# Optimization experiments

Hardware: AMD Instinct MI355X
Metric: run time of the kernel (lower is better)

The kernel has to match this reference:

```python
import jax, jax.numpy as jnp
import numpy as np

B, T, D = 2, 2048, 1024
H = 4            # num_heads (== num_kv_heads, num_kv_groups = 1)
W = 512          # window_size
S = 64           # state_size
CK = D // H      # head_k_dim = 256
CV = D // H      # head_v_dim = 256
EPS = 1e-5
SCALE = 1.0


def setup_inputs() -> dict:
    key = jax.random.key(0)
    ks = jax.random.split(key, 8)
    def w(k, o, i):
        return jax.random.normal(k, (o, i), jnp.float32) * 0.02
    return {
        "hidden_states": jax.random.normal(ks[0], (B, T, D), jnp.float32),
        "w_norm": jnp.ones((D,), jnp.float32),   # shared RMSNorm weight (pre- and post-norm; module overwrites self.norm)
        "Wq": w(ks[1], D, D),
        "Wk": w(ks[2], D, D),
        "Wv": w(ks[3], D, D),
        "Ws": w(ks[4], D, D),
        "Wg": w(ks[5], H * S, D),
        "Wo": w(ks[6], D, D),
    }


def _rms(x, w):
    return x * jax.lax.rsqrt(jnp.mean(x * x, axis=-1, keepdims=True) + EPS) * w


def reference(hidden_states, w_norm, Wq, Wk, Wv, Ws, Wg, Wo):
    h = _rms(hidden_states, w_norm)                           # pre-norm (norm_first)
    proj = lambda x, Wm: jnp.einsum('btd,od->bto', x, Wm)
    heads = lambda x, c: x.reshape(B, T, H, c).transpose(0, 2, 1, 3)
    q = heads(proj(h, Wq), CK) * SCALE                        # [B,H,T,CK]
    k = heads(proj(h, Wk), CK)
    v = heads(proj(h, Wv), CV)
    s = heads(proj(h, Ws), CK)                                # state-key projection
    g = jax.nn.softmax(proj(h, Wg), axis=-1)                  # softmax over full H*S dim (as in module)
    g = heads(g, S)                                           # [B,H,T,S] gate over state slots

    # ---- compressed global state (causal cumulative g-weighted outer products) ----
    # state_K[t] = sum_{t'<=t} g[t']^T s[t'];  scores_state[t,s] = q[t] . state_K[t,s]
    causal = jnp.tril(jnp.ones((T, T), dtype=bool))
    A = jnp.einsum('bhtc,bhuc->bhtu', q, s)                   # q . s per pair
    A = jnp.where(causal, A, 0.0)
    sc_state = jnp.einsum('bhtu,bhus->bhts', A, g)            # [B,H,T,S]

    # ---- sliding-window local attention (blocked: each query block sees prev+cur key block) ----
    nb = T // W
    qb = q.reshape(B, H, nb, W, CK)
    kb = k.reshape(B, H, nb, W, CK)
    vb = v.reshape(B, H, nb, W, CV)
    kprev = jnp.concatenate([jnp.zeros_like(kb[:, :, :1]), kb[:, :, :-1]], axis=2)
    vprev = jnp.concatenate([jnp.zeros_like(vb[:, :, :1]), vb[:, :, :-1]], axis=2)
    k2 = jnp.concatenate([kprev, kb], axis=3)                 # [B,H,nb,2W,CK]
    v2 = jnp.concatenate([vprev, vb], axis=3)                 # [B,H,nb,2W,CV]
    sc_w = jnp.einsum('bhnrc,bhnuc->bhnru', qb, k2)           # [B,H,nb,W,2W]

    r = jnp.arange(W)[:, None]
    u = jnp.arange(2 * W)[None, :]
    d = W + r - u                                             # distance t - t_key
    band = (d >= 0) & (d <= W - 1)                            # window of size W, causal
    first_blk = band & (u >= W)                               # block 0 has no real prev block
    wmask = jnp.where(jnp.arange(nb)[:, None, None] == 0, first_blk, band)   # [nb,W,2W]
    slopes = 2.0 ** (-8.0 * jnp.arange(H, dtype=jnp.float32) / H)            # [H]
    bias = -slopes[:, None, None] * d                          # alibi: slopes*(j-W+1) == -slope*dist
    sc_w = sc_w + bias[None, :, None, :, :]
    sc_w = jnp.where(wmask[None, None], sc_w, -1e30)

    # ---- joint softmax over [state ; window] columns ----
    sc = jnp.concatenate([sc_state.reshape(B, H, nb, W, S), sc_w], axis=-1)  # [B,H,nb,W,S+2W]
    p = jax.nn.softmax(sc, axis=-1)
    p_state = p[..., :S].reshape(B, H, T, S)
    p_w = p[..., S:]

    o_w = jnp.einsum('bhnru,bhnuc->bhnrc', p_w, v2).reshape(B, H, T, CV)
    # out_state[t] = sum_s p_state[t,s] * state_V[t,s],  state_V[t] = sum_{t'<=t} g[t']^T v[t']
    M = jnp.einsum('bhts,bhus->bhtu', p_state, g)
    M = jnp.where(causal, M, 0.0)
    o_s = jnp.einsum('bhtu,bhuc->bhtc', M, v)

    o = (o_w + o_s).transpose(0, 2, 1, 3).reshape(B, T, H * CV)
    o = o * jax.nn.sigmoid(o)                                  # swish
    o = _rms(o, w_norm)                                        # rms_norm_linear
    return jnp.einsum('btd,od->bto', o, Wo)
```

## Files before the change

### kernel.cpp

```cpp
#include <hip/hip_runtime.h>
#include <stdint.h>

#define B_  2
#define T_  2048
#define D_  1024
#define H_  4
#define S_  64
#define W_  512
#define CK_ 256
#define NC_ 32

typedef __attribute__((ext_vector_type(8))) short bf16x8;
typedef __attribute__((ext_vector_type(4))) float f32x4;
typedef __attribute__((ext_vector_type(4))) unsigned short u16x4;

__device__ __forceinline__ float bf2f(unsigned short u){ return __uint_as_float(((unsigned int)u)<<16); }
__device__ __forceinline__ unsigned short f2bf(float f){
  unsigned int u = __float_as_uint(f);
  u += 0x7fffu + ((u>>16)&1u);
  return (unsigned short)(u>>16);
}
__device__ __forceinline__ void split2(float y, unsigned short& hi, unsigned short& lo){
  hi = f2bf(y);
  lo = f2bf(y - bf2f(hi));
}

__device__ __forceinline__ void gl_lds16(const unsigned short* g, unsigned short* l){
  __builtin_amdgcn_global_load_lds(
      (const __attribute__((address_space(1))) unsigned int*)g,
      (__attribute__((address_space(3))) unsigned int*)l, 16, 0, 0);
}

__global__ void rmsnorm_split_kernel(const float* __restrict__ x, const float* __restrict__ w,
                                     unsigned short* __restrict__ ohi, unsigned short* __restrict__ olo){
  int row = blockIdx.x, tid = threadIdx.x;
  const float* xr = x + (size_t)row*D_;
  float v0=xr[tid], v1=xr[tid+256], v2=xr[tid+512], v3=xr[tid+768];
  __shared__ float red[256];
  red[tid] = v0*v0+v1*v1+v2*v2+v3*v3;
  __syncthreads();
  for(int s=128;s>0;s>>=1){ if(tid<s) red[tid]+=red[tid+s]; __syncthreads(); }
  float r = rsqrtf(red[0]/(float)D_ + 1e-5f);
  size_t base = (size_t)row*D_;
  float y0=v0*r*w[tid], y1=v1*r*w[tid+256], y2=v2*r*w[tid+512], y3=v3*r*w[tid+768];
  unsigned short hh, ll;
  split2(y0,hh,ll); ohi[base+tid]=hh;     olo[base+tid]=ll;
  split2(y1,hh,ll); ohi[base+tid+256]=hh; olo[base+tid+256]=ll;
  split2(y2,hh,ll); ohi[base+tid+512]=hh; olo[base+tid+512]=ll;
  split2(y3,hh,ll); ohi[base+tid+768]=hh; olo[base+tid+768]=ll;
}

__global__ void wsplit_kernel(const float* __restrict__ Wq, const float* __restrict__ Wk,
                              const float* __restrict__ Ws, const float* __restrict__ Wv,
                              const float* __restrict__ Wg, const float* __restrict__ Wo,
                              unsigned short* __restrict__ whi, unsigned short* __restrict__ wlo){
  int row = blockIdx.x, tid = threadIdx.x;
  const float* src;
  if(row < 1024)      src = Wq + (size_t)row*1024;
  else if(row < 2048) src = Wk + (size_t)(row-1024)*1024;
  else if(row < 3072) src = Ws + (size_t)(row-2048)*1024;
  else if(row < 4096) src = Wv + (size_t)(row-3072)*1024;
  else if(row < 4352) src = Wg + (size_t)(row-4096)*1024;
  else                src = Wo + (size_t)(row-4352)*1024;
  f32x4 vv = *(const f32x4*)(src + tid*4);
  u16x4 hh, ll;
  #pragma unroll
  for(int j=0;j<4;j++){ unsigned short a,b; split2(vv[j],a,b); hh[j]=a; ll[j]=b; }
  *(u16x4*)(whi + (size_t)row*1024 + tid*4) = hh;
  *(u16x4*)(wlo + (size_t)row*1024 + tid*4) = ll;
}

__global__ __launch_bounds__(256,2) void gemm_bf16s(
    const unsigned short* __restrict__ Ahi, const unsigned short* __restrict__ Alo,
    const unsigned short* __restrict__ Whi, const unsigned short* __restrict__ Wlo,
    unsigned short* __restrict__ qks, unsigned short* __restrict__ vt,
    unsigned short* __restrict__ vtlo, float* __restrict__ gout,
    float* __restrict__ Cf, int mode)
{
  __shared__ unsigned short Ah_s[128*64];
  __shared__ unsigned short Al_s[128*64];
  __shared__ unsigned short Bh_s[128*64];
  __shared__ unsigned short Bl_s[128*64];
  int tid = threadIdx.x;
  int lane = tid & 63, w = tid >> 6;
  int quad = lane >> 4, lq = lane & 15;
  int wr = w >> 1, wc = w & 1;
  int bid = blockIdx.y*gridDim.x + blockIdx.x;
  int row0, col0;
  if(mode == 0){
    int xcd = bid & 7, slot = bid >> 3;
    int rx = xcd & 3, cx = xcd >> 2;
    int sr = slot / 17, sc2 = slot % 17;
    row0 = (rx*8 + sr)*128;
    col0 = (cx*17 + sc2)*128;
  } else {
    int q8 = (gridDim.x*gridDim.y) >> 3;
    int wg = (bid & 7)*q8 + (bid >> 3);
    col0 = (wg % gridDim.x)*128;
    row0 = (wg / gridDim.x)*128;
  }

  int l8 = lane >> 3;
  int chk = lane & 7;

  f32x4 acc[4][4];
  #pragma unroll
  for(int i=0;i<4;i++)
    #pragma unroll
    for(int j=0;j<4;j++) acc[i][j] = (f32x4){0.f,0.f,0.f,0.f};

  for(int kt=0; kt<1024; kt+=64){
    __syncthreads();
    #pragma unroll
    for(int j=0;j<4;j++){
      int rl = w*32 + j*8 + l8;
      int sc = (chk ^ (rl & 7))*8;
      int lbase = (w*32 + j*8)*64;
      gl_lds16(Ahi + (size_t)(row0+rl)*1024 + kt + sc, Ah_s + lbase);
      gl_lds16(Alo + (size_t)(row0+rl)*1024 + kt + sc, Al_s + lbase);
      gl_lds16(Whi + (size_t)(col0+rl)*1024 + kt + sc, Bh_s + lbase);
      gl_lds16(Wlo + (size_t)(col0+rl)*1024 + kt + sc, Bl_s + lbase);
    }
    __syncthreads();
    #pragma unroll
    for(int ks=0;ks<2;ks++){
      bf16x8 afh[4], afl[4], bfh[4], bfl[4];
      #pragma unroll
      for(int i=0;i<4;i++){
        int Ra = wr*64+i*16+lq;
        int ca = ((ks*4+quad) ^ (Ra&7))*8;
        afh[i] = *(const bf16x8*)(const void*)(Ah_s + Ra*64 + ca);
        afl[i] = *(const bf16x8*)(const void*)(Al_s + Ra*64 + ca);
        int Rb = wc*64+i*16+lq;
        int cb = ((ks*4+quad) ^ (Rb&7))*8;
        bfh[i] = *(const bf16x8*)(const void*)(Bh_s + Rb*64 + cb);
        bfl[i] = *(const bf16x8*)(const void*)(Bl_s + Rb*64 + cb);
      }
      #pragma unroll
      for(int mi=0;mi<4;mi++)
        #pragma unroll
        for(int ni=0;ni<4;ni++){
          acc[mi][ni] = __builtin_amdgcn_mfma_f32_16x16x32_bf16(afh[mi], bfh[ni], acc[mi][ni], 0,0,0);
          acc[mi][ni] = __builtin_amdgcn_mfma_f32_16x16x32_bf16(afh[mi], bfl[ni], acc[mi][ni], 0,0,0);
          acc[mi][ni] = __builtin_amdgcn_mfma_f32_16x16x32_bf16(afl[mi], bfh[ni], acc[mi][ni], 0,0,0);
        }
    }
  }

  int rbase = row0 + wr*64, cbase = col0 + wc*64;
  if(mode == 1){
    #pragma unroll
    for(int mi=0;mi<4;mi++)
      #pragma unroll
      for(int ni=0;ni<4;ni++)
        #pragma unroll
        for(int i=0;i<4;i++)
          Cf[(size_t)(rbase+mi*16+quad*4+i)*1024 + cbase+ni*16+lq] = acc[mi][ni][i];
  } else if(col0 < 3072){
    unsigned short* dst = qks + (size_t)(col0>>10)*4194304;
    #pragma unroll
    for(int mi=0;mi<4;mi++)
      #pragma unroll
      for(int ni=0;ni<4;ni++)
        #pragma unroll
        for(int i=0;i<4;i++){
          int rr = rbase+mi*16+quad*4+i, cc = (cbase+ni*16+lq) & 1023;
          dst[(size_t)rr*1024 + cc] = f2bf(acc[mi][ni][i]);
        }
  } else if(col0 < 4096){
    #pragma unroll
    for(int mi=0;mi<4;mi++)
      #pragma unroll
      for(int ni=0;ni<4;ni++)
        #pragma unroll
        for(int i=0;i<4;i++){
          int rr = rbase+mi*16+quad*4+i, cl = (cbase+ni*16+lq) & 1023;
          unsigned short hh2, ll2;
          split2(acc[mi][ni][i], hh2, ll2);
          int hh = cl>>8, cv = cl&255, bb = rr>>11, tt = rr&2047;
          size_t ti = ((size_t)((bb*H_+hh)*256 + cv))*T_ + tt;
          vt[ti] = hh2;
          vtlo[ti] = ll2;
        }
  } else {
    #pragma unroll
    for(int mi=0;mi<4;mi++)
      #pragma unroll
      for(int ni=0;ni<4;ni++)
        #pragma unroll
        for(int i=0;i<4;i++){
          int rr = rbase+mi*16+quad*4+i, cl = cbase+ni*16+lq - 4096;
          gout[(size_t)rr*256 + cl] = acc[mi][ni][i];
        }
  }
}

__global__ void softmax256_kernel(float* __restrict__ g){
  int row = blockIdx.x, tid = threadIdx.x;
  float x = g[(size_t)row*256+tid];
  __shared__ float red[256];
  red[tid]=x; __syncthreads();
  for(int s=128;s>0;s>>=1){ if(tid<s) red[tid]=fmaxf(red[tid],red[tid+s]); __syncthreads(); }
  float m = red[0]; __syncthreads();
  float e = expf(x-m);
  red[tid]=e; __syncthreads();
  for(int s=128;s>0;s>>=1){ if(tid<s) red[tid]+=red[tid+s]; __syncthreads(); }
  g[(size_t)row*256+tid] = e/red[0];
}

__global__ __launch_bounds__(256,1) void chunk_outer_mfma(
    const unsigned short* __restrict__ gthi, const unsigned short* __restrict__ gtlo,
    const unsigned short* __restrict__ s_bf, float* __restrict__ out)
{
  __shared__ unsigned short xh_lds[256*72];
  int n=blockIdx.x, h=blockIdx.y, b=blockIdx.z;
  int tid=threadIdx.x, lane=tid&63, w=tid>>6;
  int quad=lane>>4, lq=lane&15;
  int t0=n*64, bh=b*H_+h;

  const unsigned short* sb = s_bf + (size_t)(b*T_+t0)*D_ + h*CK_ + tid;
  for(int p2=0;p2<8;p2++){
    union{ unsigned short u[8]; bf16x8 v8; } r8;
    #pragma unroll
    for(int j=0;j<8;j++)
      r8.u[j] = sb[(size_t)(p2*8+j)*D_];
    *(bf16x8*)(void*)&xh_lds[tid*72 + p2*8] = r8.v8;
  }
  __syncthreads();

  size_t gtbase = ((size_t)bh*NC_ + n)*64;
  f32x4 acc[4][4];
  #pragma unroll
  for(int i=0;i<4;i++)
    #pragma unroll
    for(int j=0;j<4;j++) acc[i][j] = (f32x4){0.f,0.f,0.f,0.f};

  #pragma unroll
  for(int ks=0; ks<2; ks++){
    bf16x8 ah[4], al[4], bh4[4];
    #pragma unroll
    for(int mi=0;mi<4;mi++){
      ah[mi] = *(const bf16x8*)(const void*)(gthi + (gtbase + mi*16+lq)*64 + ks*32 + quad*8);
      al[mi] = *(const bf16x8*)(const void*)(gtlo + (gtbase + mi*16+lq)*64 + ks*32 + quad*8);
    }
    #pragma unroll
    for(int ni=0;ni<4;ni++)
      bh4[ni] = *(const bf16x8*)(const void*)&xh_lds[(w*64+ni*16+lq)*72 + ks*32 + quad*8];
    #pragma unroll
    for(int mi=0;mi<4;mi++)
      #pragma unroll
      for(int ni=0;ni<4;ni++){
        acc[mi][ni] = __builtin_amdgcn_mfma_f32_16x16x32_bf16(ah[mi], bh4[ni], acc[mi][ni], 0,0,0);
        acc[mi][ni] = __builtin_amdgcn_mfma_f32_16x16x32_bf16(al[mi], bh4[ni], acc[mi][ni], 0,0,0);
      }
  }
  size_t obase = ((size_t)bh*NC_ + n)*16384;
  #pragma unroll
  for(int mi=0;mi<4;mi++)
    #pragma unroll
    for(int ni=0;ni<4;ni++)
      #pragma unroll
      for(int i=0;i<4;i++){
        int s = mi*16 + quad*4 + i, c = w*64 + ni*16 + lq;
        out[obase + (size_t)s*256 + c] = acc[mi][ni][i];
      }
}

__global__ __launch_bounds__(256,1) void chunk_outer_vt(
    const unsigned short* __restrict__ gthi, const unsigned short* __restrict__ gtlo,
    const unsigned short* __restrict__ vt, const unsigned short* __restrict__ vtlo,
    float* __restrict__ out)
{
  int n=blockIdx.x, h=blockIdx.y, b=blockIdx.z;
  int tid=threadIdx.x, lane=tid&63, w=tid>>6;
  int quad=lane>>4, lq=lane&15;
  int t0=n*64, bh=b*H_+h;
  size_t gtbase = ((size_t)bh*NC_ + n)*64;
  f32x4 acc[4][4];
  #pragma unroll
  for(int i=0;i<4;i++)
    #pragma unroll
    for(int j=0;j<4;j++) acc[i][j] = (f32x4){0.f,0.f,0.f,0.f};

  #pragma unroll
  for(int ks=0; ks<2; ks++){
    bf16x8 ah[4], al[4];
    #pragma unroll
    for(int mi=0;mi<4;mi++){
      ah[mi] = *(const bf16x8*)(const void*)(gthi + (gtbase + mi*16+lq)*64 + ks*32 + quad*8);
      al[mi] = *(const bf16x8*)(const void*)(gtlo + (gtbase + mi*16+lq)*64 + ks*32 + quad*8);
    }
    #pragma unroll
    for(int ni=0;ni<4;ni++){
      size_t vo = ((size_t)(bh*256 + w*64 + ni*16 + lq))*T_ + t0 + ks*32 + quad*8;
      bf16x8 vh = *(const bf16x8*)(const void*)(vt + vo);
      bf16x8 vl = *(const bf16x8*)(const void*)(vtlo + vo);
      #pragma unroll
      for(int mi=0;mi<4;mi++){
        acc[mi][ni] = __builtin_amdgcn_mfma_f32_16x16x32_bf16(ah[mi], vh, acc[mi][ni], 0,0,0);
        acc[mi][ni] = __builtin_amdgcn_mfma_f32_16x16x32_bf16(al[mi], vh, acc[mi][ni], 0,0,0);
        acc[mi][ni] = __builtin_amdgcn_mfma_f32_16x16x32_bf16(ah[mi], vl, acc[mi][ni], 0,0,0);
      }
    }
  }
  size_t obase = ((size_t)bh*NC_ + n)*16384;
  #pragma unroll
  for(int mi=0;mi<4;mi++)
    #pragma unroll
    for(int ni=0;ni<4;ni++){
      int c = w*64 + ni*16 + lq, s0 = mi*16 + quad*4;
      *(f32x4*)&out[obase + (size_t)c*64 + s0] = acc[mi][ni];
    }
}

__global__ void chunk_prefix_split_kernel(const float* __restrict__ arr,
    unsigned short* __restrict__ hi, unsigned short* __restrict__ lo){
  int idx = blockIdx.x*256 + threadIdx.x;
  int bh = idx >> 14, e = idx & 16383;
  float run = 0.f;
  size_t base = (size_t)bh*NC_*16384 + e;
  for(int n=0;n<NC_;n++){
    size_t a = base + (size_t)n*16384;
    float t = arr[a];
    unsigned short hh, ll;
    split2(run, hh, ll);
    hi[a] = hh; lo[a] = ll;
    run += t;
  }
}

__global__ __launch_bounds__(256) void g_transpose_split_kernel(const float* __restrict__ g,
    unsigned short* __restrict__ gthi, unsigned short* __restrict__ gtlo){
  int n=blockIdx.x, h=blockIdx.y, b=blockIdx.z;
  int tid=threadIdx.x, t0=n*64;
  __shared__ float tt[64][65];
  #pragma unroll
  for(int p=0;p<16;p++){
    int u = (tid>>6) + p*4, s = tid&63;
    tt[s][u] = g[((size_t)(b*T_ + t0 + u))*256 + h*64 + s];
  }
  __syncthreads();
  size_t base = ((size_t)(b*H_+h)*NC_ + n)*64;
  #pragma unroll
  for(int p=0;p<16;p++){
    int s = (tid>>6) + p*4, u = tid&63;
    unsigned short hh, ll;
    split2(tt[s][u], hh, ll);
    gthi[(base+s)*64 + u] = hh;
    gtlo[(base+s)*64 + u] = ll;
  }
}

__global__ __launch_bounds__(256,1) void sc_state_mfma(
    const unsigned short* __restrict__ q_bf,
    const unsigned short* __restrict__ s_bf,
    const unsigned short* __restrict__ S1hi, const unsigned short* __restrict__ S1lo,
    const unsigned short* __restrict__ gthi, const unsigned short* __restrict__ gtlo,
    float* __restrict__ sc_state)
{
  int n=blockIdx.x, h=blockIdx.y, b=blockIdx.z;
  int tid=threadIdx.x, lane=tid&63, w=tid>>6;
  int quad=lane>>4, lq=lane&15;
  int t0=n*64, bh=b*H_+h, strip=w*16;

  __shared__ unsigned short A_hi[64*72];
  __shared__ unsigned short A_lo[64*72];

  bf16x8 qf[8];
  const unsigned short* qrow = q_bf + ((size_t)(b*T_ + t0 + strip + lq))*D_ + h*CK_ + quad*8;
  #pragma unroll
  for(int ks=0;ks<8;ks++) qf[ks] = *(const bf16x8*)(const void*)(qrow + ks*32);

  const unsigned short* sbase = s_bf + ((size_t)(b*T_ + t0))*D_ + h*CK_;
  f32x4 a1[4];
  #pragma unroll
  for(int nf=0;nf<4;nf++) a1[nf] = (f32x4){0.f,0.f,0.f,0.f};
  #pragma unroll
  for(int ks=0;ks<8;ks++){
    #pragma unroll
    for(int nf=0;nf<4;nf++){
      bf16x8 sf = *(const bf16x8*)(const void*)(sbase + (size_t)(nf*16+lq)*D_ + ks*32 + quad*8);
      a1[nf] = __builtin_amdgcn_mfma_f32_16x16x32_bf16(qf[ks], sf, a1[nf], 0,0,0);
    }
  }
  #pragma unroll
  for(int nf=0;nf<4;nf++){
    int u = nf*16 + lq;
    #pragma unroll
    for(int i=0;i<4;i++){
      int trow = strip + quad*4 + i;
      float val = (u <= trow) ? a1[nf][i] : 0.f;
      unsigned short hh, ll;
      split2(val, hh, ll);
      A_hi[trow*72 + u] = hh;
      A_lo[trow*72 + u] = ll;
    }
  }
  __syncthreads();

  bf16x8 afh[2], afl[2];
  #pragma unroll
  for(int ks=0;ks<2;ks++){
    afh[ks] = *(const bf16x8*)(const void*)&A_hi[(strip+lq)*72 + ks*32 + quad*8];
    afl[ks] = *(const bf16x8*)(const void*)&A_lo[(strip+lq)*72 + ks*32 + quad*8];
  }

  size_t s1base = ((size_t)bh*NC_ + n)*16384;
  size_t gtbase = ((size_t)bh*NC_ + n)*64;
  f32x4 acc2[4];
  #pragma unroll
  for(int nf=0;nf<4;nf++) acc2[nf] = (f32x4){0.f,0.f,0.f,0.f};
  #pragma unroll
  for(int ks=0;ks<8;ks++){
    #pragma unroll
    for(int nf=0;nf<4;nf++){
      size_t off = s1base + (size_t)(nf*16+lq)*256 + ks*32 + quad*8;
      bf16x8 b1 = *(const bf16x8*)(const void*)(S1hi + off);
      acc2[nf] = __builtin_amdgcn_mfma_f32_16x16x32_bf16(qf[ks], b1, acc2[nf], 0,0,0);
      bf16x8 b2 = *(const bf16x8*)(const void*)(S1lo + off);
      acc2[nf] = __builtin_amdgcn_mfma_f32_16x16x32_bf16(qf[ks], b2, acc2[nf], 0,0,0);
    }
  }
  #pragma unroll
  for(int ks=0;ks<2;ks++){
    #pragma unroll
    for(int nf=0;nf<4;nf++){
      size_t off = (gtbase + nf*16+lq)*64 + ks*32 + quad*8;
      bf16x8 gh = *(const bf16x8*)(const void*)(gthi + off);
      bf16x8 gl = *(const bf16x8*)(const void*)(gtlo + off);
      acc2[nf] = __builtin_amdgcn_mfma_f32_16x16x32_bf16(afh[ks], gh, acc2[nf], 0,0,0);
      acc2[nf] = __builtin_amdgcn_mfma_f32_16x16x32_bf16(afh[ks], gl, acc2[nf], 0,0,0);
      acc2[nf] = __builtin_amdgcn_mfma_f32_16x16x32_bf16(afl[ks], gh, acc2[nf], 0,0,0);
    }
  }
  #pragma unroll
  for(int nf=0;nf<4;nf++){
    #pragma unroll
    for(int i=0;i<4;i++){
      int trow = strip + quad*4 + i;
      sc_state[((size_t)bh*T_ + t0 + trow)*64 + nf*16+lq] = acc2[nf][i];
    }
  }
}

__global__ __launch_bounds__(256,1) void window_attn_mfma(
    const unsigned short* __restrict__ q_bf,
    const unsigned short* __restrict__ k_bf,
    const unsigned short* __restrict__ vt_bf,
    const float* __restrict__ sc_state,
    float* __restrict__ o,
    unsigned short* __restrict__ phi, unsigned short* __restrict__ plo)
{
  int nt=blockIdx.x, h=blockIdx.y, b=blockIdx.z;
  int tid=threadIdx.x;
  int lane = tid & 63, w = tid >> 6;
  int quad = lane >> 4, lq = lane & 15;
  int sp = w >> 1, np = w & 1;
  int t0 = nt*64, bh = b*H_ + h;
  float slope = exp2f(-2.0f*(float)h);

  __shared__ unsigned short kv_lds[256*72];
  __shared__ float S_lds[64*68];
  __shared__ unsigned short P_lds[64*72];
  __shared__ float m_lds[64], l_lds[64], al_lds[64];

  bf16x8 qf[2][8];
  #pragma unroll
  for(int st=0; st<2; st++){
    const unsigned short* qrow = q_bf + ((size_t)(b*T_ + t0 + 32*sp + 16*st + lq))*D_ + h*CK_ + quad*8;
    #pragma unroll
    for(int ks=0; ks<8; ks++)
      qf[st][ks] = *(const bf16x8*)(const void*)(qrow + ks*32);
  }

  int jt0 = (nt>=8)? nt-8 : 0;
  int krow = tid>>2, kseg = tid&3;
  bf16x8 kpre[8];
  {
    const unsigned short* src = k_bf + ((size_t)(b*T_ + jt0*64 + krow))*D_ + h*CK_ + kseg*64;
    #pragma unroll
    for(int i=0;i<8;i++) kpre[i] = *(const bf16x8*)(const void*)(src + i*8);
  }

  int r = tid >> 2, part = tid & 3;
  {
    const float* scrow = sc_state + ((size_t)bh*T_ + t0 + r)*64 + part*16;
    float pm = -1e30f, sv[16];
    #pragma unroll
    for(int i=0;i<16;i++){ sv[i] = scrow[i]; pm = fmaxf(pm, sv[i]); }
    pm = fmaxf(pm, __shfl_xor(pm,1)); pm = fmaxf(pm, __shfl_xor(pm,2));
    float ps = 0.f;
    #pragma unroll
    for(int i=0;i<16;i++) ps += __expf(sv[i]-pm);
    ps += __shfl_xor(ps,1); ps += __shfl_xor(ps,2);
    if(part==0){ m_lds[r]=pm; l_lds[r]=ps; }
  }

  f32x4 o_acc[2][8];
  #pragma unroll
  for(int st=0;st<2;st++)
    #pragma unroll
    for(int nv=0;nv<8;nv++) o_acc[st][nv] = (f32x4){0.f,0.f,0.f,0.f};
  __syncthreads();

  for(int jt=jt0; jt<=nt; jt++){
    int j0 = jt*64;
    {
      unsigned short* dst = kv_lds + krow*260 + kseg*64;
      #pragma unroll
      for(int i=0;i<8;i++) *(bf16x8*)(void*)(dst + i*8) = kpre[i];
    }
    __syncthreads();
    if(jt < nt){
      const unsigned short* src = k_bf + ((size_t)(b*T_ + j0 + 64 + krow))*D_ + h*CK_ + kseg*64;
      #pragma unroll
      for(int i=0;i<8;i++) kpre[i] = *(const bf16x8*)(const void*)(src + i*8);
    }
    f32x4 sacc[2][2];
    #pragma unroll
    for(int st=0;st<2;st++)
      #pragma unroll
      for(int n2=0;n2<2;n2++) sacc[st][n2] = (f32x4){0.f,0.f,0.f,0.f};
    #pragma unroll
    for(int n2=0;n2<2;n2++){
      int n = np*2 + n2;
      #pragma unroll
      for(int ks=0;ks<8;ks++){
        bf16x8 kf = *(const bf16x8*)(const void*)(kv_lds + (n*16+lq)*260 + ks*32 + quad*8);
        sacc[0][n2] = __builtin_amdgcn_mfma_f32_16x16x32_bf16(qf[0][ks], kf, sacc[0][n2], 0,0,0);
        sacc[1][n2] = __builtin_amdgcn_mfma_f32_16x16x32_bf16(qf[1][ks], kf, sacc[1][n2], 0,0,0);
      }
    }
    #pragma unroll
    for(int st=0;st<2;st++){
      #pragma unroll
      for(int n2=0;n2<2;n2++){
        int n = np*2+n2;
        int u = j0 + n*16 + lq;
        #pragma unroll
        for(int i=0;i<4;i++){
          int row = 32*sp + 16*st + quad*4 + i;
          int d = (t0 + row) - u;
          float val = (d>=0 && d<W_) ? sacc[st][n2][i] - slope*(float)d : -1e30f;
          S_lds[row*68 + n*16+lq] = val;
        }
      }
    }
    __syncthreads();
    {
      float s16[16], tm = -1e30f;
      #pragma unroll
      for(int i=0;i<16;i++){ s16[i] = S_lds[r*68 + part*16 + i]; tm = fmaxf(tm, s16[i]); }
      tm = fmaxf(tm, __shfl_xor(tm,1)); tm = fmaxf(tm, __shfl_xor(tm,2));
      float m_old = m_lds[r];
      float m_new = fmaxf(m_old, tm);
      float alpha = __expf(m_old - m_new);
      float ts = 0.f;
      union { unsigned short u[16]; bf16x8 v[2]; } pk;
      #pragma unroll
      for(int i=0;i<16;i++){ float p = __expf(s16[i]-m_new); ts += p; pk.u[i] = f2bf(p); }
      ts += __shfl_xor(ts,1); ts += __shfl_xor(ts,2);
      *(bf16x8*)(void*)&P_lds[r*72 + part*16]     = pk.v[0];
      *(bf16x8*)(void*)&P_lds[r*72 + part*16 + 8] = pk.v[1];
      if(part==0){ m_lds[r] = m_new; l_lds[r] = l_lds[r]*alpha + ts; al_lds[r] = alpha; }
      #pragma unroll
      for(int pass=0; pass<4; pass++){
        int cv = (tid>>2) + 64*pass, useg = (tid&3)*16;
        const unsigned short* src = vt_bf + ((size_t)(bh*256 + cv))*T_ + j0 + useg;
        unsigned short* dst = kv_lds + cv*72 + useg;
        *(bf16x8*)(void*)(dst)   = *(const bf16x8*)(const void*)(src);
        *(bf16x8*)(void*)(dst+8) = *(const bf16x8*)(const void*)(src+8);
      }
    }
    __syncthreads();
    #pragma unroll
    for(int st=0;st<2;st++){
      #pragma unroll
      for(int i=0;i<4;i++){
        float al = al_lds[32*sp+16*st+quad*4+i];
        #pragma unroll
        for(int nv=0;nv<8;nv++) o_acc[st][nv][i] *= al;
      }
    }
    bf16x8 pa[2][2];
    #pragma unroll
    for(int st=0;st<2;st++)
      #pragma unroll
      for(int k2=0;k2<2;k2++)
        pa[st][k2] = *(const bf16x8*)(const void*)&P_lds[(32*sp+16*st+lq)*72 + k2*32 + quad*8];
    #pragma unroll
    for(int nv=0;nv<8;nv++){
      int cvt = np*8 + nv;
      #pragma unroll
      for(int k2=0;k2<2;k2++){
        bf16x8 vb = *(const bf16x8*)(const void*)(kv_lds + (cvt*16+lq)*72 + k2*32 + quad*8);
        o_acc[0][nv] = __builtin_amdgcn_mfma_f32_16x16x32_bf16(pa[0][k2], vb, o_acc[0][nv], 0,0,0);
        o_acc[1][nv] = __builtin_amdgcn_mfma_f32_16x16x32_bf16(pa[1][k2], vb, o_acc[1][nv], 0,0,0);
      }
    }
    __syncthreads();
  }
  #pragma unroll
  for(int st=0;st<2;st++){
    #pragma unroll
    for(int i=0;i<4;i++){
      int row = 32*sp+16*st+quad*4+i;
      float rl = 1.0f / l_lds[row];
      #pragma unroll
      for(int nv=0;nv<8;nv++){
        int cv = (np*8+nv)*16 + lq;
        o[((size_t)bh*T_ + t0 + row)*256 + cv] = o_acc[st][nv][i] * rl;
      }
    }
  }
  {
    float mf = m_lds[r], rlf = 1.0f / l_lds[r];
    const float* scrow = sc_state + ((size_t)bh*T_ + t0 + r)*64 + part*16;
    size_t pb = ((size_t)bh*T_ + t0 + r)*64 + part*16;
    #pragma unroll
    for(int i=0;i<16;i++){
      float pv = __expf(scrow[i]-mf)*rlf;
      unsigned short hh, ll;
      split2(pv, hh, ll);
      phi[pb+i] = hh;
      plo[pb+i] = ll;
    }
  }
}

__global__ __launch_bounds__(256,1) void o_state_mfma(
    const unsigned short* __restrict__ phi, const unsigned short* __restrict__ plo,
    const float* __restrict__ g,
    const unsigned short* __restrict__ S2hi, const unsigned short* __restrict__ S2lo,
    const unsigned short* __restrict__ vt, const unsigned short* __restrict__ vtlo,
    float* __restrict__ o)
{
  __shared__ unsigned short gh_lds[64*72];
  __shared__ unsigned short gl_lds[64*72];
  __shared__ unsigned short Mh_lds[64*72];
  __shared__ unsigned short Ml_lds[64*72];
  int n=blockIdx.x, h=blockIdx.y, b=blockIdx.z;
  int tid=threadIdx.x, lane=tid&63, w=tid>>6;
  int quad=lane>>4, lq=lane&15;
  int t0=n*64, bh=b*H_+h, strip=w*16;

  {
    int gu = tid>>2, gs0 = (tid&3)*16;
    const float* gr = g + ((size_t)(b*T_+t0+gu))*256 + h*64 + gs0;
    union{ unsigned short u[16]; bf16x8 v[2]; } GH, GL;
    #pragma unroll
    for(int j=0;j<16;j++) split2(gr[j], GH.u[j], GL.u[j]);
    *(bf16x8*)(void*)&gh_lds[gu*72+gs0]   = GH.v[0];
    *(bf16x8*)(void*)&gh_lds[gu*72+gs0+8] = GH.v[1];
    *(bf16x8*)(void*)&gl_lds[gu*72+gs0]   = GL.v[0];
    *(bf16x8*)(void*)&gl_lds[gu*72+gs0+8] = GL.v[1];
  }
  __syncthreads();

  {
    const unsigned short* ph = phi + ((size_t)bh*T_ + t0 + strip + lq)*64;
    const unsigned short* pl = plo + ((size_t)bh*T_ + t0 + strip + lq)*64;
    f32x4 ma[4];
    #pragma unroll
    for(int nf=0;nf<4;nf++) ma[nf] = (f32x4){0.f,0.f,0.f,0.f};
    #pragma unroll
    for(int ks=0;ks<2;ks++){
      bf16x8 pfh = *(const bf16x8*)(const void*)(ph + ks*32 + quad*8);
      bf16x8 pfl = *(const bf16x8*)(const void*)(pl + ks*32 + quad*8);
      #pragma unroll
      for(int nf=0;nf<4;nf++){
        bf16x8 gH = *(const bf16x8*)(const void*)&gh_lds[(nf*16+lq)*72 + ks*32 + quad*8];
        bf16x8 gL = *(const bf16x8*)(const void*)&gl_lds[(nf*16+lq)*72 + ks*32 + quad*8];
        ma[nf] = __builtin_amdgcn_mfma_f32_16x16x32_bf16(pfh, gH, ma[nf], 0,0,0);
        ma[nf] = __builtin_amdgcn_mfma_f32_16x16x32_bf16(pfh, gL, ma[nf], 0,0,0);
        ma[nf] = __builtin_amdgcn_mfma_f32_16x16x32_bf16(pfl, gH, ma[nf], 0,0,0);
      }
    }
    #pragma unroll
    for(int nf=0;nf<4;nf++){
      int u = nf*16 + lq;
      #pragma unroll
      for(int i=0;i<4;i++){
        int trow = strip + quad*4 + i;
        float val = (u <= trow) ? ma[nf][i] : 0.f;
        unsigned short hh, ll;
        split2(val, hh, ll);
        Mh_lds[trow*72 + u] = hh;
        Ml_lds[trow*72 + u] = ll;
      }
    }
  }
  __syncthreads();

  f32x4 oacc[4][4];
  #pragma unroll
  for(int i=0;i<4;i++)
    #pragma unroll
    for(int j=0;j<4;j++) oacc[i][j] = (f32x4){0.f,0.f,0.f,0.f};
  int c0 = w*64;
  size_t sgbase = ((size_t)bh*NC_ + n)*16384;
  #pragma unroll
  for(int ks=0;ks<2;ks++){
    bf16x8 pAh[4], pAl[4], mAh[4], mAl[4];
    #pragma unroll
    for(int mi=0;mi<4;mi++){
      size_t po = ((size_t)bh*T_ + t0 + mi*16+lq)*64 + ks*32 + quad*8;
      pAh[mi] = *(const bf16x8*)(const void*)(phi + po);
      pAl[mi] = *(const bf16x8*)(const void*)(plo + po);
      mAh[mi] = *(const bf16x8*)(const void*)&Mh_lds[(mi*16+lq)*72 + ks*32 + quad*8];
      mAl[mi] = *(const bf16x8*)(const void*)&Ml_lds[(mi*16+lq)*72 + ks*32 + quad*8];
    }
    #pragma unroll
    for(int ni=0;ni<4;ni++){
      int c = c0 + ni*16 + lq;
      size_t so = sgbase + (size_t)c*64 + ks*32 + quad*8;
      bf16x8 sgH = *(const bf16x8*)(const void*)(S2hi + so);
      bf16x8 sgL = *(const bf16x8*)(const void*)(S2lo + so);
      size_t vo = ((size_t)(bh*256 + c))*T_ + t0 + ks*32 + quad*8;
      bf16x8 vH = *(const bf16x8*)(const void*)(vt + vo);
      bf16x8 vL = *(const bf16x8*)(const void*)(vtlo + vo);
      #pragma unroll
      for(int mi=0;mi<4;mi++){
        oacc[mi][ni] = __builtin_amdgcn_mfma_f32_16x16x32_bf16(pAh[mi], sgH, oacc[mi][ni], 0,0,0);
        oacc[mi][ni] = __builtin_amdgcn_mfma_f32_16x16x32_bf16(pAh[mi], sgL, oacc[mi][ni], 0,0,0);
        oacc[mi][ni] = __builtin_amdgcn_mfma_f32_16x16x32_bf16(pAl[mi], sgH, oacc[mi][ni], 0,0,0);
        oacc[mi][ni] = __builtin_amdgcn_mfma_f32_16x16x32_bf16(mAh[mi], vH, oacc[mi][ni], 0,0,0);
        oacc[mi][ni] = __builtin_amdgcn_mfma_f32_16x16x32_bf16(mAl[mi], vH, oacc[mi][ni], 0,0,0);
        oacc[mi][ni] = __builtin_amdgcn_mfma_f32_16x16x32_bf16(mAh[mi], vL, oacc[mi][ni], 0,0,0);
      }
    }
  }
  #pragma unroll
  for(int mi=0;mi<4;mi++)
    #pragma unroll
    for(int ni=0;ni<4;ni++)
      #pragma unroll
      for(int i=0;i<4;i++){
        int trow = mi*16 + quad*4 + i, c = c0 + ni*16 + lq;
        size_t oi = ((size_t)bh*T_ + t0 + trow)*256 + c;
        o[oi] += oacc[mi][ni][i];
      }
}

__global__ void swish_rms_split_kernel(const float* __restrict__ o, const float* __restrict__ w,
                                       unsigned short* __restrict__ ohi, unsigned short* __restrict__ olo){
  int bt=blockIdx.x, tid=threadIdx.x;
  int b = bt >> 11, t = bt & 2047;
  float y[4]; float ss=0.f;
  #pragma unroll
  for(int hh=0;hh<4;hh++){
    float x = o[((size_t)(b*H_+hh)*T_ + t)*256 + tid];
    float yy = x / (1.f + expf(-x));
    y[hh]=yy; ss += yy*yy;
  }
  __shared__ float red[256];
  red[tid]=ss; __syncthreads();
  for(int s2=128;s2>0;s2>>=1){ if(tid<s2) red[tid]+=red[tid+s2]; __syncthreads(); }
  float r = rsqrtf(red[0]/1024.f + 1e-5f);
  #pragma unroll
  for(int hh=0;hh<4;hh++){
    unsigned short a,bq;
    split2(y[hh]*r*w[hh*256+tid], a, bq);
    ohi[(size_t)bt*1024 + hh*256 + tid] = a;
    olo[(size_t)bt*1024 + hh*256 + tid] = bq;
  }
}

extern "C" void kernel_launch(void* const* d_in, const int* in_sizes, int n_in,
                              void* d_out, int out_size, void* d_ws, size_t ws_size,
                              hipStream_t stream){
  const float* hidden = (const float*)d_in[0];
  const float* w_norm = (const float*)d_in[1];
  const float* Wq = (const float*)d_in[2];
  const float* Wk = (const float*)d_in[3];
  const float* Wv = (const float*)d_in[4];
  const float* Ws = (const float*)d_in[5];
  const float* Wg = (const float*)d_in[6];
  const float* Wo = (const float*)d_in[7];
  float* out = (float*)d_out;

  char* p = (char*)d_ws;
  auto alloc = [&](size_t bytes)->void*{ void* r = (void*)p; p += (bytes + 255) & ~(size_t)255; return r; };
  unsigned short* h_hi = (unsigned short*)alloc(8388608);
  unsigned short* h_lo = (unsigned short*)alloc(8388608);
  unsigned short* Wc_hi = (unsigned short*)alloc(11010048);
  unsigned short* Wc_lo = (unsigned short*)alloc(11010048);
  unsigned short* vslot = (unsigned short*)alloc(16777216);
  float* g   = (float*)alloc(4194304);
  float* P1  = (float*)alloc(16777216);
  float* P2  = (float*)alloc(16777216);
  float* sc  = (float*)alloc(4194304);
  float* ps  = (float*)alloc(4194304);
  unsigned short* qks = (unsigned short*)alloc(25165824);
  unsigned short* vt  = (unsigned short*)alloc(8388608);

  unsigned short* vtlo = vslot;
  unsigned short* S2hi = vslot + 4194304;
  unsigned short* q_bf = qks;
  unsigned short* k_bf = qks + 4194304;
  unsigned short* s_bf = qks + 8388608;
  unsigned short* S2lo = s_bf;
  float* o = P1;
  unsigned short* S1hi = (unsigned short*)P2;
  unsigned short* S1lo = S1hi + 4194304;
  unsigned short* GThi = (unsigned short*)ps;
  unsigned short* GTlo = GThi + 1048576;
  unsigned short* phi  = (unsigned short*)ps;
  unsigned short* plo  = phi + 1048576;

  rmsnorm_split_kernel<<<4096,256,0,stream>>>(hidden, w_norm, h_hi, h_lo);
  wsplit_kernel<<<5376,256,0,stream>>>(Wq, Wk, Ws, Wv, Wg, Wo, Wc_hi, Wc_lo);
  gemm_bf16s<<<dim3(34,32),256,0,stream>>>(h_hi, h_lo, Wc_hi, Wc_lo,
                                           qks, vt, vtlo, g, nullptr, 0);
  softmax256_kernel<<<4096,256,0,stream>>>(g);
  dim3 gc(32,4,2);
  g_transpose_split_kernel<<<gc,256,0,stream>>>(g, GThi, GTlo);
  chunk_outer_mfma<<<gc,256,0,stream>>>(GThi, GTlo, s_bf, P1);
  chunk_prefix_split_kernel<<<512,256,0,stream>>>(P1, S1hi, S1lo);
  sc_state_mfma<<<gc,256,0,stream>>>(q_bf, s_bf, S1hi, S1lo, GThi, GTlo, sc);
  chunk_outer_vt<<<gc,256,0,stream>>>(GThi, GTlo, vt, vtlo, P2);
  chunk_prefix_split_kernel<<<512,256,0,stream>>>(P2, S2hi, S2lo);
  window_attn_mfma<<<gc,256,0,stream>>>(q_bf, k_bf, vt, sc, o, phi, plo);
  o_state_mfma<<<gc,256,0,stream>>>(phi, plo, g, S2hi, S2lo, vt, vtlo, o);
  swish_rms_split_kernel<<<4096,256,0,stream>>>(o, w_norm, h_hi, h_lo);
  gemm_bf16s<<<dim3(8,32),256,0,stream>>>(h_hi, h_lo, Wc_hi + (size_t)4352*1024, Wc_lo + (size_t)4352*1024,
                                          nullptr, nullptr, nullptr, nullptr, out, 1);
}
```

Before: 384.6 us.

## Fuse pre-norm/weight split, softmax/transpose, chunk outers, and window/state output kernels

Merges the RMSNorm and weight-split kernels into one launch, folds the gate transpose and hi/lo split into the softmax kernel, and computes both chunk outer products (s and v) in a single kernel. The state-output computation moves into the window-attention kernel, so the state probabilities stay in LDS and are added to the window accumulators in registers instead of going through a global round trip and a read-modify-write of o. This removes several launches and intermediate global buffers, at the cost of much more LDS per block in the fused attention kernel and a strided, uncoalesced transposed store from the softmax kernel.

```diff
diff --git a/kernel.cpp b/kernel.cpp
--- a/kernel.cpp
+++ b/kernel.cpp
@@ -31,43 +31,45 @@
       (__attribute__((address_space(3))) unsigned int*)l, 16, 0, 0);
 }
 
-__global__ void rmsnorm_split_kernel(const float* __restrict__ x, const float* __restrict__ w,
-                                     unsigned short* __restrict__ ohi, unsigned short* __restrict__ olo){
-  int row = blockIdx.x, tid = threadIdx.x;
-  const float* xr = x + (size_t)row*D_;
-  float v0=xr[tid], v1=xr[tid+256], v2=xr[tid+512], v3=xr[tid+768];
-  __shared__ float red[256];
-  red[tid] = v0*v0+v1*v1+v2*v2+v3*v3;
-  __syncthreads();
-  for(int s=128;s>0;s>>=1){ if(tid<s) red[tid]+=red[tid+s]; __syncthreads(); }
-  float r = rsqrtf(red[0]/(float)D_ + 1e-5f);
-  size_t base = (size_t)row*D_;
-  float y0=v0*r*w[tid], y1=v1*r*w[tid+256], y2=v2*r*w[tid+512], y3=v3*r*w[tid+768];
-  unsigned short hh, ll;
-  split2(y0,hh,ll); ohi[base+tid]=hh;     olo[base+tid]=ll;
-  split2(y1,hh,ll); ohi[base+tid+256]=hh; olo[base+tid+256]=ll;
-  split2(y2,hh,ll); ohi[base+tid+512]=hh; olo[base+tid+512]=ll;
-  split2(y3,hh,ll); ohi[base+tid+768]=hh; olo[base+tid+768]=ll;
-}
-
-__global__ void wsplit_kernel(const float* __restrict__ Wq, const float* __restrict__ Wk,
-                              const float* __restrict__ Ws, const float* __restrict__ Wv,
-                              const float* __restrict__ Wg, const float* __restrict__ Wo,
-                              unsigned short* __restrict__ whi, unsigned short* __restrict__ wlo){
-  int row = blockIdx.x, tid = threadIdx.x;
-  const float* src;
-  if(row < 1024)      src = Wq + (size_t)row*1024;
-  else if(row < 2048) src = Wk + (size_t)(row-1024)*1024;
-  else if(row < 3072) src = Ws + (size_t)(row-2048)*1024;
-  else if(row < 4096) src = Wv + (size_t)(row-3072)*1024;
-  else if(row < 4352) src = Wg + (size_t)(row-4096)*1024;
-  else                src = Wo + (size_t)(row-4352)*1024;
-  f32x4 vv = *(const f32x4*)(src + tid*4);
-  u16x4 hh, ll;
-  #pragma unroll
-  for(int j=0;j<4;j++){ unsigned short a,b; split2(vv[j],a,b); hh[j]=a; ll[j]=b; }
-  *(u16x4*)(whi + (size_t)row*1024 + tid*4) = hh;
-  *(u16x4*)(wlo + (size_t)row*1024 + tid*4) = ll;
+__global__ void norm_wsplit_kernel(const float* __restrict__ x, const float* __restrict__ w,
+                                   unsigned short* __restrict__ ohi, unsigned short* __restrict__ olo,
+                                   const float* __restrict__ Wq, const float* __restrict__ Wk,
+                                   const float* __restrict__ Ws, const float* __restrict__ Wv,
+                                   const float* __restrict__ Wg, const float* __restrict__ Wo,
+                                   unsigned short* __restrict__ whi, unsigned short* __restrict__ wlo){
+  int tid = threadIdx.x;
+  if(blockIdx.x < 4096){
+    int row = blockIdx.x;
+    const float* xr = x + (size_t)row*D_;
+    float v0=xr[tid], v1=xr[tid+256], v2=xr[tid+512], v3=xr[tid+768];
+    __shared__ float red[256];
+    red[tid] = v0*v0+v1*v1+v2*v2+v3*v3;
+    __syncthreads();
+    for(int s=128;s>0;s>>=1){ if(tid<s) red[tid]+=red[tid+s]; __syncthreads(); }
+    float r = rsqrtf(red[0]/(float)D_ + 1e-5f);
+    size_t base = (size_t)row*D_;
+    float y0=v0*r*w[tid], y1=v1*r*w[tid+256], y2=v2*r*w[tid+512], y3=v3*r*w[tid+768];
+    unsigned short hh, ll;
+    split2(y0,hh,ll); ohi[base+tid]=hh;     olo[base+tid]=ll;
+    split2(y1,hh,ll); ohi[base+tid+256]=hh; olo[base+tid+256]=ll;
+    split2(y2,hh,ll); ohi[base+tid+512]=hh; olo[base+tid+512]=ll;
+    split2(y3,hh,ll); ohi[base+tid+768]=hh; olo[base+tid+768]=ll;
+  } else {
+    int row = blockIdx.x - 4096;
+    const float* src;
+    if(row < 1024)      src = Wq + (size_t)row*1024;
+    else if(row < 2048) src = Wk + (size_t)(row-1024)*1024;
+    else if(row < 3072) src = Ws + (size_t)(row-2048)*1024;
+    else if(row < 4096) src = Wv + (size_t)(row-3072)*1024;
+    else if(row < 4352) src = Wg + (size_t)(row-4096)*1024;
+    else                src = Wo + (size_t)(row-4352)*1024;
+    f32x4 vv = *(const f32x4*)(src + tid*4);
+    u16x4 hh, ll;
+    #pragma unroll
+    for(int j=0;j<4;j++){ unsigned short a,b2; split2(vv[j],a,b2); hh[j]=a; ll[j]=b2; }
+    *(u16x4*)(whi + (size_t)row*1024 + tid*4) = hh;
+    *(u16x4*)(wlo + (size_t)row*1024 + tid*4) = ll;
+  }
 }
 
 __global__ __launch_bounds__(256,2) void gemm_bf16s(
@@ -195,7 +197,8 @@
   }
 }
 
-__global__ void softmax256_kernel(float* __restrict__ g){
+__global__ void softmax256_gt_kernel(float* __restrict__ g,
+    unsigned short* __restrict__ gthi, unsigned short* __restrict__ gtlo){
   int row = blockIdx.x, tid = threadIdx.x;
   float x = g[(size_t)row*256+tid];
   __shared__ float red[256];
@@ -205,18 +208,31 @@
   float e = expf(x-m);
   red[tid]=e; __syncthreads();
   for(int s=128;s>0;s>>=1){ if(tid<s) red[tid]+=red[tid+s]; __syncthreads(); }
-  g[(size_t)row*256+tid] = e/red[0];
-}
-
-__global__ __launch_bounds__(256,1) void chunk_outer_mfma(
+  float val = e/red[0];
+  g[(size_t)row*256+tid] = val;
+  int b = row >> 11, t = row & 2047;
+  int n = t >> 6, u = t & 63;
+  int hsel = tid >> 6, s = tid & 63;
+  unsigned short hh, ll;
+  split2(val, hh, ll);
+  size_t base = ((size_t)(b*H_+hsel)*NC_ + n)*64;
+  gthi[(base+s)*64 + u] = hh;
+  gtlo[(base+s)*64 + u] = ll;
+}
+
+__global__ __launch_bounds__(256,1) void chunk_outer_both(
     const unsigned short* __restrict__ gthi, const unsigned short* __restrict__ gtlo,
-    const unsigned short* __restrict__ s_bf, float* __restrict__ out)
+    const unsigned short* __restrict__ s_bf,
+    const unsigned short* __restrict__ vt, const unsigned short* __restrict__ vtlo,
+    float* __restrict__ outS, float* __restrict__ outV)
 {
   __shared__ unsigned short xh_lds[256*72];
   int n=blockIdx.x, h=blockIdx.y, b=blockIdx.z;
   int tid=threadIdx.x, lane=tid&63, w=tid>>6;
   int quad=lane>>4, lq=lane&15;
   int t0=n*64, bh=b*H_+h;
+  size_t gtbase = ((size_t)bh*NC_ + n)*64;
+  size_t obase = ((size_t)bh*NC_ + n)*16384;
 
   const unsigned short* sb = s_bf + (size_t)(b*T_+t0)*D_ + h*CK_ + tid;
   for(int p2=0;p2<8;p2++){
@@ -228,13 +244,11 @@
   }
   __syncthreads();
 
-  size_t gtbase = ((size_t)bh*NC_ + n)*64;
   f32x4 acc[4][4];
   #pragma unroll
   for(int i=0;i<4;i++)
     #pragma unroll
     for(int j=0;j<4;j++) acc[i][j] = (f32x4){0.f,0.f,0.f,0.f};
-
   #pragma unroll
   for(int ks=0; ks<2; ks++){
     bf16x8 ah[4], al[4], bh4[4];
@@ -254,7 +268,6 @@
         acc[mi][ni] = __builtin_amdgcn_mfma_f32_16x16x32_bf16(al[mi], bh4[ni], acc[mi][ni], 0,0,0);
       }
   }
-  size_t obase = ((size_t)bh*NC_ + n)*16384;
   #pragma unroll
   for(int mi=0;mi<4;mi++)
     #pragma unroll
@@ -262,26 +275,13 @@
       #pragma unroll
       for(int i=0;i<4;i++){
         int s = mi*16 + quad*4 + i, c = w*64 + ni*16 + lq;
-        out[obase + (size_t)s*256 + c] = acc[mi][ni][i];
-      }
-}
-
-__global__ __launch_bounds__(256,1) void chunk_outer_vt(
-    const unsigned short* __restrict__ gthi, const unsigned short* __restrict__ gtlo,
-    const unsigned short* __restrict__ vt, const unsigned short* __restrict__ vtlo,
-    float* __restrict__ out)
-{
-  int n=blockIdx.x, h=blockIdx.y, b=blockIdx.z;
-  int tid=threadIdx.x, lane=tid&63, w=tid>>6;
-  int quad=lane>>4, lq=lane&15;
-  int t0=n*64, bh=b*H_+h;
-  size_t gtbase = ((size_t)bh*NC_ + n)*64;
-  f32x4 acc[4][4];
+        outS[obase + (size_t)s*256 + c] = acc[mi][ni][i];
+      }
+
   #pragma unroll
   for(int i=0;i<4;i++)
     #pragma unroll
     for(int j=0;j<4;j++) acc[i][j] = (f32x4){0.f,0.f,0.f,0.f};
-
   #pragma unroll
   for(int ks=0; ks<2; ks++){
     bf16x8 ah[4], al[4];
@@ -303,13 +303,12 @@
       }
     }
   }
-  size_t obase = ((size_t)bh*NC_ + n)*16384;
   #pragma unroll
   for(int mi=0;mi<4;mi++)
     #pragma unroll
     for(int ni=0;ni<4;ni++){
       int c = w*64 + ni*16 + lq, s0 = mi*16 + quad*4;
-      *(f32x4*)&out[obase + (size_t)c*64 + s0] = acc[mi][ni];
+      *(f32x4*)&outV[obase + (size_t)c*64 + s0] = acc[mi][ni];
     }
 }
 
@@ -329,28 +328,6 @@
   }
 }
 
-__global__ __launch_bounds__(256) void g_transpose_split_kernel(const float* __restrict__ g,
-    unsigned short* __restrict__ gthi, unsigned short* __restrict__ gtlo){
-  int n=blockIdx.x, h=blockIdx.y, b=blockIdx.z;
-  int tid=threadIdx.x, t0=n*64;
-  __shared__ float tt[64][65];
-  #pragma unroll
-  for(int p=0;p<16;p++){
-    int u = (tid>>6) + p*4, s = tid&63;
-    tt[s][u] = g[((size_t)(b*T_ + t0 + u))*256 + h*64 + s];
-  }
-  __syncthreads();
-  size_t base = ((size_t)(b*H_+h)*NC_ + n)*64;
-  #pragma unroll
-  for(int p=0;p<16;p++){
-    int s = (tid>>6) + p*4, u = tid&63;
-    unsigned short hh, ll;
-    split2(tt[s][u], hh, ll);
-    gthi[(base+s)*64 + u] = hh;
-    gtlo[(base+s)*64 + u] = ll;
-  }
-}
-
 __global__ __launch_bounds__(256,1) void sc_state_mfma(
     const unsigned short* __restrict__ q_bf,
     const unsigned short* __restrict__ s_bf,
@@ -443,13 +420,15 @@
   }
 }
 
-__global__ __launch_bounds__(256,1) void window_attn_mfma(
+__global__ __launch_bounds__(256,1) void window_attn_state_mfma(
     const unsigned short* __restrict__ q_bf,
     const unsigned short* __restrict__ k_bf,
     const unsigned short* __restrict__ vt_bf,
+    const unsigned short* __restrict__ vtlo_bf,
     const float* __restrict__ sc_state,
-    float* __restrict__ o,
-    unsigned short* __restrict__ phi, unsigned short* __restrict__ plo)
+    const float* __restrict__ g,
+    const unsigned short* __restrict__ S2hi, const unsigned short* __restrict__ S2lo,
+    float* __restrict__ o)
 {
   int nt=blockIdx.x, h=blockIdx.y, b=blockIdx.z;
   int tid=threadIdx.x;
@@ -462,6 +441,11 @@
   __shared__ unsigned short kv_lds[256*72];
   __shared__ float S_lds[64*68];
   __shared__ unsigned short P_lds[64*72];
+  __shared__ unsigned short Pl_lds[64*72];
+  __shared__ unsigned short gh_lds[64*72];
+  __shared__ unsigned short gl_lds[64*72];
+  __shared__ unsigned short Mh_lds[64*72];
+  __shared__ unsigned short Ml_lds[64*72];
   __shared__ float m_lds[64], l_lds[64], al_lds[64];
 
   bf16x8 qf[2][8];
@@ -600,50 +584,30 @@
     }
     __syncthreads();
   }
-  #pragma unroll
-  for(int st=0;st<2;st++){
+
+  #pragma unroll
+  for(int st=0;st<2;st++)
     #pragma unroll
     for(int i=0;i<4;i++){
       int row = 32*sp+16*st+quad*4+i;
       float rl = 1.0f / l_lds[row];
       #pragma unroll
-      for(int nv=0;nv<8;nv++){
-        int cv = (np*8+nv)*16 + lq;
-        o[((size_t)bh*T_ + t0 + row)*256 + cv] = o_acc[st][nv][i] * rl;
-      }
-    }
-  }
+      for(int nv=0;nv<8;nv++) o_acc[st][nv][i] *= rl;
+    }
   {
     float mf = m_lds[r], rlf = 1.0f / l_lds[r];
     const float* scrow = sc_state + ((size_t)bh*T_ + t0 + r)*64 + part*16;
-    size_t pb = ((size_t)bh*T_ + t0 + r)*64 + part*16;
+    union { unsigned short u[16]; bf16x8 v[2]; } PH, PL;
     #pragma unroll
     for(int i=0;i<16;i++){
       float pv = __expf(scrow[i]-mf)*rlf;
-      unsigned short hh, ll;
-      split2(pv, hh, ll);
-      phi[pb+i] = hh;
-      plo[pb+i] = ll;
-    }
-  }
-}
-
-__global__ __launch_bounds__(256,1) void o_state_mfma(
-    const unsigned short* __restrict__ phi, const unsigned short* __restrict__ plo,
-    const float* __restrict__ g,
-    const unsigned short* __restrict__ S2hi, const unsigned short* __restrict__ S2lo,
-    const unsigned short* __restrict__ vt, const unsigned short* __restrict__ vtlo,
-    float* __restrict__ o)
-{
-  __shared__ unsigned short gh_lds[64*72];
-  __shared__ unsigned short gl_lds[64*72];
-  __shared__ unsigned short Mh_lds[64*72];
-  __shared__ unsigned short Ml_lds[64*72];
-  int n=blockIdx.x, h=blockIdx.y, b=blockIdx.z;
-  int tid=threadIdx.x, lane=tid&63, w=tid>>6;
-  int quad=lane>>4, lq=lane&15;
-  int t0=n*64, bh=b*H_+h, strip=w*16;
-
+      split2(pv, PH.u[i], PL.u[i]);
+    }
+    *(bf16x8*)(void*)&P_lds[r*72 + part*16]      = PH.v[0];
+    *(bf16x8*)(void*)&P_lds[r*72 + part*16 + 8]  = PH.v[1];
+    *(bf16x8*)(void*)&Pl_lds[r*72 + part*16]     = PL.v[0];
+    *(bf16x8*)(void*)&Pl_lds[r*72 + part*16 + 8] = PL.v[1];
+  }
   {
     int gu = tid>>2, gs0 = (tid&3)*16;
     const float* gr = g + ((size_t)(b*T_+t0+gu))*256 + h*64 + gs0;
@@ -658,15 +622,14 @@
   __syncthreads();
 
   {
-    const unsigned short* ph = phi + ((size_t)bh*T_ + t0 + strip + lq)*64;
-    const unsigned short* pl = plo + ((size_t)bh*T_ + t0 + strip + lq)*64;
+    int strip = w*16;
     f32x4 ma[4];
     #pragma unroll
     for(int nf=0;nf<4;nf++) ma[nf] = (f32x4){0.f,0.f,0.f,0.f};
     #pragma unroll
     for(int ks=0;ks<2;ks++){
-      bf16x8 pfh = *(const bf16x8*)(const void*)(ph + ks*32 + quad*8);
-      bf16x8 pfl = *(const bf16x8*)(const void*)(pl + ks*32 + quad*8);
+      bf16x8 pfh = *(const bf16x8*)(const void*)&P_lds[(strip+lq)*72 + ks*32 + quad*8];
+      bf16x8 pfl = *(const bf16x8*)(const void*)&Pl_lds[(strip+lq)*72 + ks*32 + quad*8];
       #pragma unroll
       for(int nf=0;nf<4;nf++){
         bf16x8 gH = *(const bf16x8*)(const void*)&gh_lds[(nf*16+lq)*72 + ks*32 + quad*8];
@@ -692,54 +655,50 @@
   }
   __syncthreads();
 
-  f32x4 oacc[4][4];
-  #pragma unroll
-  for(int i=0;i<4;i++)
-    #pragma unroll
-    for(int j=0;j<4;j++) oacc[i][j] = (f32x4){0.f,0.f,0.f,0.f};
-  int c0 = w*64;
-  size_t sgbase = ((size_t)bh*NC_ + n)*16384;
+  size_t sgbase = ((size_t)bh*NC_ + nt)*16384;
   #pragma unroll
   for(int ks=0;ks<2;ks++){
-    bf16x8 pAh[4], pAl[4], mAh[4], mAl[4];
-    #pragma unroll
-    for(int mi=0;mi<4;mi++){
-      size_t po = ((size_t)bh*T_ + t0 + mi*16+lq)*64 + ks*32 + quad*8;
-      pAh[mi] = *(const bf16x8*)(const void*)(phi + po);
-      pAl[mi] = *(const bf16x8*)(const void*)(plo + po);
-      mAh[mi] = *(const bf16x8*)(const void*)&Mh_lds[(mi*16+lq)*72 + ks*32 + quad*8];
-      mAl[mi] = *(const bf16x8*)(const void*)&Ml_lds[(mi*16+lq)*72 + ks*32 + quad*8];
-    }
-    #pragma unroll
-    for(int ni=0;ni<4;ni++){
-      int c = c0 + ni*16 + lq;
+    bf16x8 pAh[2], pAl[2], mAh[2], mAl[2];
+    #pragma unroll
+    for(int st=0;st<2;st++){
+      int rowb = (32*sp + 16*st + lq)*72 + ks*32 + quad*8;
+      pAh[st] = *(const bf16x8*)(const void*)&P_lds[rowb];
+      pAl[st] = *(const bf16x8*)(const void*)&Pl_lds[rowb];
+      mAh[st] = *(const bf16x8*)(const void*)&Mh_lds[rowb];
+      mAl[st] = *(const bf16x8*)(const void*)&Ml_lds[rowb];
+    }
+    #pragma unroll
+    for(int nv=0;nv<8;nv++){
+      int c = (np*8+nv)*16 + lq;
       size_t so = sgbase + (size_t)c*64 + ks*32 + quad*8;
       bf16x8 sgH = *(const bf16x8*)(const void*)(S2hi + so);
       bf16x8 sgL = *(const bf16x8*)(const void*)(S2lo + so);
       size_t vo = ((size_t)(bh*256 + c))*T_ + t0 + ks*32 + quad*8;
-      bf16x8 vH = *(const bf16x8*)(const void*)(vt + vo);
-      bf16x8 vL = *(const bf16x8*)(const void*)(vtlo + vo);
-      #pragma unroll
-      for(int mi=0;mi<4;mi++){
-        oacc[mi][ni] = __builtin_amdgcn_mfma_f32_16x16x32_bf16(pAh[mi], sgH, oacc[mi][ni], 0,0,0);
-        oacc[mi][ni] = __builtin_amdgcn_mfma_f32_16x16x32_bf16(pAh[mi], sgL, oacc[mi][ni], 0,0,0);
-        oacc[mi][ni] = __builtin_amdgcn_mfma_f32_16x16x32_bf16(pAl[mi], sgH, oacc[mi][ni], 0,0,0);
-        oacc[mi][ni] = __builtin_amdgcn_mfma_f32_16x16x32_bf16(mAh[mi], vH, oacc[mi][ni], 0,0,0);
-        oacc[mi][ni] = __builtin_amdgcn_mfma_f32_16x16x32_bf16(mAl[mi], vH, oacc[mi][ni], 0,0,0);
-        oacc[mi][ni] = __builtin_amdgcn_mfma_f32_16x16x32_bf16(mAh[mi], vL, oacc[mi][ni], 0,0,0);
-      }
-    }
-  }
-  #pragma unroll
-  for(int mi=0;mi<4;mi++)
-    #pragma unroll
-    for(int ni=0;ni<4;ni++)
-      #pragma unroll
-      for(int i=0;i<4;i++){
-        int trow = mi*16 + quad*4 + i, c = c0 + ni*16 + lq;
-        size_t oi = ((size_t)bh*T_ + t0 + trow)*256 + c;
-        o[oi] += oacc[mi][ni][i];
-      }
+      bf16x8 vH = *(const bf16x8*)(const void*)(vt_bf + vo);
+      bf16x8 vL = *(const bf16x8*)(const void*)(vtlo_bf + vo);
+      #pragma unroll
+      for(int st=0;st<2;st++){
+        o_acc[st][nv] = __builtin_amdgcn_mfma_f32_16x16x32_bf16(pAh[st], sgH, o_acc[st][nv], 0,0,0);
+        o_acc[st][nv] = __builtin_amdgcn_mfma_f32_16x16x32_bf16(pAh[st], sgL, o_acc[st][nv], 0,0,0);
+        o_acc[st][nv] = __builtin_amdgcn_mfma_f32_16x16x32_bf16(pAl[st], sgH, o_acc[st][nv], 0,0,0);
+        o_acc[st][nv] = __builtin_amdgcn_mfma_f32_16x16x32_bf16(mAh[st], vH, o_acc[st][nv], 0,0,0);
+        o_acc[st][nv] = __builtin_amdgcn_mfma_f32_16x16x32_bf16(mAl[st], vH, o_acc[st][nv], 0,0,0);
+        o_acc[st][nv] = __builtin_amdgcn_mfma_f32_16x16x32_bf16(mAh[st], vL, o_acc[st][nv], 0,0,0);
+      }
+    }
+  }
+  #pragma unroll
+  for(int st=0;st<2;st++){
+    #pragma unroll
+    for(int i=0;i<4;i++){
+      int row = 32*sp+16*st+quad*4+i;
+      #pragma unroll
+      for(int nv=0;nv<8;nv++){
+        int cv = (np*8+nv)*16 + lq;
+        o[((size_t)bh*T_ + t0 + row)*256 + cv] = o_acc[st][nv][i];
+      }
+    }
+  }
 }
 
 __global__ void swish_rms_split_kernel(const float* __restrict__ o, const float* __restrict__ w,
@@ -801,27 +760,23 @@
   unsigned short* s_bf = qks + 8388608;
   unsigned short* S2lo = s_bf;
   float* o = P1;
+  float* P2f = (float*)h_hi;
   unsigned short* S1hi = (unsigned short*)P2;
   unsigned short* S1lo = S1hi + 4194304;
   unsigned short* GThi = (unsigned short*)ps;
   unsigned short* GTlo = GThi + 1048576;
-  unsigned short* phi  = (unsigned short*)ps;
-  unsigned short* plo  = phi + 1048576;
-
-  rmsnorm_split_kernel<<<4096,256,0,stream>>>(hidden, w_norm, h_hi, h_lo);
-  wsplit_kernel<<<5376,256,0,stream>>>(Wq, Wk, Ws, Wv, Wg, Wo, Wc_hi, Wc_lo);
+
+  norm_wsplit_kernel<<<9472,256,0,stream>>>(hidden, w_norm, h_hi, h_lo,
+                                            Wq, Wk, Ws, Wv, Wg, Wo, Wc_hi, Wc_lo);
   gemm_bf16s<<<dim3(34,32),256,0,stream>>>(h_hi, h_lo, Wc_hi, Wc_lo,
                                            qks, vt, vtlo, g, nullptr, 0);
-  softmax256_kernel<<<4096,256,0,stream>>>(g);
+  softmax256_gt_kernel<<<4096,256,0,stream>>>(g, GThi, GTlo);
   dim3 gc(32,4,2);
-  g_transpose_split_kernel<<<gc,256,0,stream>>>(g, GThi, GTlo);
-  chunk_outer_mfma<<<gc,256,0,stream>>>(GThi, GTlo, s_bf, P1);
+  chunk_outer_both<<<gc,256,0,stream>>>(GThi, GTlo, s_bf, vt, vtlo, P1, P2f);
   chunk_prefix_split_kernel<<<512,256,0,stream>>>(P1, S1hi, S1lo);
   sc_state_mfma<<<gc,256,0,stream>>>(q_bf, s_bf, S1hi, S1lo, GThi, GTlo, sc);
-  chunk_outer_vt<<<gc,256,0,stream>>>(GThi, GTlo, vt, vtlo, P2);
-  chunk_prefix_split_kernel<<<512,256,0,stream>>>(P2, S2hi, S2lo);
-  window_attn_mfma<<<gc,256,0,stream>>>(q_bf, k_bf, vt, sc, o, phi, plo);
-  o_state_mfma<<<gc,256,0,stream>>>(phi, plo, g, S2hi, S2lo, vt, vtlo, o);
+  chunk_prefix_split_kernel<<<512,256,0,stream>>>(P2f, S2hi, S2lo);
+  window_attn_state_mfma<<<gc,256,0,stream>>>(q_bf, k_bf, vt, vtlo, sc, g, S2hi, S2lo, o);
   swish_rms_split_kernel<<<4096,256,0,stream>>>(o, w_norm, h_hi, h_lo);
   gemm_bf16s<<<dim3(8,32),256,0,stream>>>(h_hi, h_lo, Wc_hi + (size_t)4352*1024, Wc_lo + (size_t)4352*1024,
                                           nullptr, nullptr, nullptr, nullptr, out, 1);
```

After: 377.3 us (median of 2 runs). No clear change (-1.9%).
